# Kernel optimization log

Measured on AMD Instinct MI355X. Metric: run time of the kernel, lower is better.

Reference implementation:

```python
import jax, jax.numpy as jnp
import numpy as np

N = 8192
PERCEPTION = 0.2
SEP_DIST = 0.02
ACC_SCALE = 1.0
ACC_MAX = 1.0
EPS = 1e-08


def setup_inputs() -> dict:
    key = jax.random.key(0)
    k1, k2, k3 = jax.random.split(key, 3)
    position = jax.random.uniform(k1, (N, 2), dtype=jnp.float32)  # boids live in [0,1]^2 torus
    velocity = jax.random.normal(k2, (N, 2), dtype=jnp.float32) * 0.05
    noise = jax.random.uniform(k3, (N, 2), dtype=jnp.float32, minval=-1.0, maxval=1.0)
    return {
        "position": position,
        "velocity": velocity,
        "noise": noise,
        "separation_weight": jnp.float32(4.5),
        "alignment_weight": jnp.float32(0.65),
        "cohesion_weight": jnp.float32(0.75),
        "noise_scale": jnp.float32(0.05),
    }


def _normalize(v):
    # per-row normalize, matching module's _normalize
    norm = jnp.maximum(jnp.linalg.norm(v, axis=-1, keepdims=True), EPS)
    return v / norm


def reference(position, velocity, noise, separation_weight, alignment_weight, cohesion_weight, noise_scale):
    # Toroidal vector from boid i to boid j: diff[i, j, :]  (shape [N, N, 2])
    diff = position[None, :, :] - position[:, None, :]
    diff = jnp.where(diff > 0.5, diff - 1.0, diff)
    diff = jnp.where(diff < -0.5, diff + 1.0, diff)
    dist2 = jnp.sum(diff * diff, axis=-1)  # [N, N]

    not_self = ~jnp.eye(N, dtype=bool)

    # Separation: sum of -toroidal_vector over too-close neighbors, normalized
    sep_mask = not_self & (dist2 <= SEP_DIST ** 2)
    steer_sep = -jnp.sum(jnp.where(sep_mask[..., None], diff, 0.0), axis=1)
    steer_sep = _normalize(steer_sep)

    # Perception mask shared by alignment and cohesion
    perc_mask = not_self & (dist2 <= PERCEPTION ** 2)
    cnt = jnp.sum(perc_mask, axis=1, dtype=position.dtype)[:, None]  # [N, 1]

    # Alignment: mean neighbor velocity minus own velocity, normalized
    vel_avg = jnp.einsum("ij,jd->id", perc_mask.astype(position.dtype), velocity) / cnt
    steer_align = _normalize(vel_avg - velocity)

    # Cohesion: mean toroidal vector to neighbors, normalized
    pos_avg = jnp.sum(jnp.where(perc_mask[..., None], diff, 0.0), axis=1) / cnt
    steer_coh = _normalize(pos_avg)

    acc = (separation_weight * steer_sep
           + alignment_weight * steer_align
           + cohesion_weight * steer_coh)
    acc = acc * ACC_SCALE
    acc = acc + noise_scale * noise

    # clip by norm per boid
    norm = jnp.linalg.norm(acc, axis=-1, keepdims=True)
    acc = jnp.where(norm > ACC_MAX, acc * ACC_MAX / jnp.maximum(norm, EPS), acc)
    return acc
```

## Files before the change

### kernel.cpp

```cpp
#include <hip/hip_runtime.h>
#include <math.h>

#define N_BOIDS 8192
typedef float f32x2 __attribute__((ext_vector_type(2)));
typedef float f32x4 __attribute__((ext_vector_type(4)));

constexpr int   NC     = 16;
constexpr int   NCELL  = NC * NC;
constexpr float MARG   = 0.2002f;
constexpr int   CHUNK  = 256;
constexpr int   NBLK   = N_BOIDS / CHUNK;
constexpr size_t HIST_OFF = 0;
constexpr size_t CS_OFF   = 32768;
constexpr size_t SORT_OFF = 36864;
constexpr size_t SIDX_OFF = 167936;
constexpr size_t WS_NEED  = 200704;

constexpr float SEP_R2  = 4.0000000000000008e-04f;
constexpr float PERC_R2 = 4.0000000000000001e-02f;
constexpr float EPSF    = 1e-08f;

__device__ __forceinline__ int cell_of(float px, float py) {
    int cx = (int)(px * 16.0f); cx = cx > 15 ? 15 : (cx < 0 ? 0 : cx);
    int cy = (int)(py * 16.0f); cy = cy > 15 ? 15 : (cy < 0 ? 0 : cy);
    return cy * NC + cx;
}

__global__ __launch_bounds__(CHUNK) void cell_hist(
    const float* __restrict__ pos, int* __restrict__ hist)
{
    __shared__ int h[NCELL];
    const int tid = threadIdx.x;
    h[tid] = 0;
    __syncthreads();
    const int i = blockIdx.x * CHUNK + tid;
    atomicAdd(&h[cell_of(pos[2 * i], pos[2 * i + 1])], 1);
    __syncthreads();
    hist[blockIdx.x * NCELL + tid] = h[tid];
}

__global__ __launch_bounds__(CHUNK) void cell_scan_scatter(
    const float* __restrict__ pos, const float* __restrict__ vel,
    const int* __restrict__ hist, int* __restrict__ cs,
    float4* __restrict__ sorted4, int* __restrict__ sidx)
{
    __shared__ int tot[NCELL];
    __shared__ int lbase[NCELL];
    __shared__ int cid[CHUNK];
    const int c = threadIdx.x;
    const int b = blockIdx.x;

    int t = 0, part = 0;
#pragma unroll
    for (int bb = 0; bb < NBLK; ++bb) {
        const int hv = hist[bb * NCELL + c];
        t += hv;
        if (bb < b) part += hv;
    }
    const int mytot = t;
    tot[c] = t;
    __syncthreads();
#pragma unroll
    for (int off = 1; off < NCELL; off <<= 1) {
        int v = 0;
        if (c >= off) v = tot[c - off];
        __syncthreads();
        tot[c] += v;
        __syncthreads();
    }
    const int excl = tot[c] - mytot;
    lbase[c] = excl + part;
    cs[c] = excl;
    if (c == NCELL - 1) cs[NCELL] = tot[NCELL - 1];

    const int i = b * CHUNK + c;
    const float px = pos[2 * i], py = pos[2 * i + 1];
    const int myc = cell_of(px, py);
    cid[c] = myc;
    __syncthreads();
    int rank = 0;
    for (int t2 = 0; t2 < c; ++t2) rank += (cid[t2] == myc) ? 1 : 0;
    const int slot = lbase[myc] + rank;
    float4 o; o.x = px; o.y = py; o.z = vel[2 * i]; o.w = vel[2 * i + 1];
    sorted4[slot] = o;
    sidx[slot]    = i;
}

__device__ __forceinline__ void finalize_core(
    float vix, float viy, const f32x2 nz,
    float ws, float wa, float wc, float wn,
    float sx, float sy, float vx, float vy, float cx, float cy, float cntall,
    float* __restrict__ out, int orig)
{
    const float cnt = cntall - 1.0f;
    float ns  = fmaxf(sqrtf(sx * sx + sy * sy), EPSF);
    float ssx = sx / ns, ssy = sy / ns;
    float vax = (vx - vix) / cnt - vix;
    float vay = (vy - viy) / cnt - viy;
    float na  = fmaxf(sqrtf(vax * vax + vay * vay), EPSF);
    float sax = vax / na, say = vay / na;
    float pax = cx / cnt, pay = cy / cnt;
    float nc  = fmaxf(sqrtf(pax * pax + pay * pay), EPSF);
    float scx = pax / nc, scy = pay / nc;
    float ax = ws * ssx + wa * sax + wc * scx;
    float ay = ws * ssy + wa * say + wc * scy;
    ax += wn * nz.x;
    ay += wn * nz.y;
    const float nn = sqrtf(ax * ax + ay * ay);
    if (nn > 1.0f) {
        const float s = 1.0f / fmaxf(nn, EPSF);
        ax *= s;
        ay *= s;
    }
    out[2 * orig]     = ax;
    out[2 * orig + 1] = ay;
}

__global__ __launch_bounds__(256, 8) void boids_main(
    const float4* __restrict__ sorted4,
    const int* __restrict__ sidx,
    const int* __restrict__ cs,
    const f32x2* __restrict__ noise,
    const float* __restrict__ w_sep,
    const float* __restrict__ w_ali,
    const float* __restrict__ w_coh,
    const float* __restrict__ w_noise,
    float* __restrict__ out)
{
    __shared__ int cs_l[NCELL + 1];
    const int tid = threadIdx.x;
    cs_l[tid] = cs[tid];
    if (tid == 0) cs_l[NCELL] = cs[NCELL];
    __syncthreads();

    const int lane = tid & 63;
    const int wid  = tid >> 6;
    const int si   = blockIdx.x * 4 + wid;

    const float4 I0 = sorted4[si];
    const float vperc = PERC_R2;
    const float vsep  = SEP_R2;

    const int cx0 = (int)floorf((I0.x - MARG) * 16.0f);
    const int cx1 = (int)floorf((I0.x + MARG) * 16.0f);
    const int cy0 = (int)floorf((I0.y - MARG) * 16.0f);
    const int cy1 = (int)floorf((I0.y + MARG) * 16.0f);
    int nx = cx1 - cx0 + 1; if (nx > NC) nx = NC;
    int ny = cy1 - cy0 + 1; if (ny > NC) ny = NC;
    const int a0 = cx0 & (NC - 1);
    const int lenA = (nx < NC - a0) ? nx : (NC - a0);
    const int lenB = nx - lenA;

    float n0 = 0.f, s0x = 0.f, s0y = 0.f, v0x = 0.f, v0y = 0.f, c0x = 0.f, c0y = 0.f;

    for (int r = 0; r < ny; ++r) {
        const int ry      = (cy0 + r) & (NC - 1);
        const int rowbase = ry * NC;
        const int sA = cs_l[rowbase + a0];
        const int eA = cs_l[rowbase + a0 + lenA];
        const int sB = cs_l[rowbase];
        const int eB = cs_l[rowbase + lenB];
        for (int seg = 0; seg < 2; ++seg) {
            const int js = seg ? sB : sA;
            const int je = seg ? eB : eA;
            for (int j0 = js; j0 < je; j0 += 64) {
                const int   rem = je - j0;
                const int   jj  = (lane < rem) ? (j0 + lane) : j0;
                const float inv = (lane < rem) ? 0.0f : 1e9f;
                const float4 q  = sorted4[jj];
                float dx, dy, ta, tb, m;
                asm(
                    "v_sub_f32   %[dx], %[qx], %[px]\n\t"
                    "v_sub_f32   %[dy], %[qy], %[py]\n\t"
                    "v_rndne_f32 %[ta], %[dx]\n\t"
                    "v_rndne_f32 %[tb], %[dy]\n\t"
                    "v_sub_f32   %[dx], %[dx], %[ta]\n\t"
                    "v_sub_f32   %[dy], %[dy], %[tb]\n\t"
                    "v_mul_f32   %[ta], %[dx], %[dx]\n\t"
                    "v_mul_f32   %[tb], %[dy], %[dy]\n\t"
                    "v_add_f32   %[ta], %[ta], %[tb]\n\t"
                    "v_max_f32   %[ta], %[ta], %[inv]\n\t"
                    "v_cmp_ge_f32 vcc, %[vperc], %[ta]\n\t"
                    "v_cndmask_b32 %[m], 0, 1.0, vcc\n\t"
                    "v_add_f32   %[n0], %[n0], %[m]\n\t"
                    "v_fmac_f32  %[v0x], %[m], %[qz]\n\t"
                    "v_fmac_f32  %[v0y], %[m], %[qw]\n\t"
                    "v_fmac_f32  %[c0x], %[m], %[dx]\n\t"
                    "v_fmac_f32  %[c0y], %[m], %[dy]\n\t"
                    "v_cmp_ge_f32 vcc, %[vsep], %[ta]\n\t"
                    "v_cndmask_b32 %[m], 0, 1.0, vcc\n\t"
                    "v_fma_f32   %[s0x], -%[m], %[dx], %[s0x]\n\t"
                    "v_fma_f32   %[s0y], -%[m], %[dy], %[s0y]\n\t"
                    : [dx] "=&v"(dx), [dy] "=&v"(dy), [ta] "=&v"(ta),
                      [tb] "=&v"(tb), [m] "=&v"(m),
                      [n0] "+v"(n0), [s0x] "+v"(s0x), [s0y] "+v"(s0y),
                      [v0x] "+v"(v0x), [v0y] "+v"(v0y),
                      [c0x] "+v"(c0x), [c0y] "+v"(c0y)
                    : [qx] "v"(q.x), [qy] "v"(q.y), [qz] "v"(q.z), [qw] "v"(q.w),
                      [px] "v"(I0.x), [py] "v"(I0.y),
                      [vperc] "v"(vperc), [vsep] "v"(vsep), [inv] "v"(inv)
                    : "vcc");
            }
        }
    }

#pragma unroll
    for (int mlev = 1; mlev < 64; mlev <<= 1) {
        n0  += __shfl_xor(n0,  mlev);
        s0x += __shfl_xor(s0x, mlev);  s0y += __shfl_xor(s0y, mlev);
        v0x += __shfl_xor(v0x, mlev);  v0y += __shfl_xor(v0y, mlev);
        c0x += __shfl_xor(c0x, mlev);  c0y += __shfl_xor(c0y, mlev);
    }

    if (lane == 0) {
        const int orig = sidx[si];
        finalize_core(I0.z, I0.w, noise[orig],
                      w_sep[0], w_ali[0], w_coh[0], w_noise[0],
                      s0x, s0y, v0x, v0y, c0x, c0y, n0, out, orig);
    }
}

constexpr int FB_BLOCK = 256;
constexpr int FB_TILE  = 2048;

__global__ __launch_bounds__(FB_BLOCK, 4) void boids_allpairs(
    const f32x2* __restrict__ pos, const f32x2* __restrict__ vel,
    const f32x2* __restrict__ noise,
    const float* __restrict__ w_sep, const float* __restrict__ w_ali,
    const float* __restrict__ w_coh, const float* __restrict__ w_noise,
    float* __restrict__ out)
{
    __shared__ f32x4 tile[FB_TILE];
    const int tid  = threadIdx.x;
    const int lane = tid & 63;
    const int wid  = tid >> 6;
    const int i0   = (blockIdx.x * 4 + wid) * 2;
    const f32x2 P0 = pos[i0];
    const f32x2 P1 = pos[i0 + 1];
    const float vperc = PERC_R2, vsep = SEP_R2;
    float n0 = 0.f, s0x = 0.f, s0y = 0.f, v0x = 0.f, v0y = 0.f, c0x = 0.f, c0y = 0.f;
    float n1 = 0.f, s1x = 0.f, s1y = 0.f, v1x = 0.f, v1y = 0.f, c1x = 0.f, c1y = 0.f;
    for (int t = 0; t < N_BOIDS / FB_TILE; ++t) {
        const f32x4* gp = reinterpret_cast<const f32x4*>(pos) + t * (FB_TILE / 2);
        const f32x4* gv = reinterpret_cast<const f32x4*>(vel) + t * (FB_TILE / 2);
#pragma unroll
        for (int c = 0; c < FB_TILE / 2 / FB_BLOCK; ++c) {
            const int idx  = tid + c * FB_BLOCK;
            const f32x4 pp = gp[idx];
            const f32x4 vv = gv[idx];
            f32x4 t0; t0.x = pp.x; t0.y = pp.y; t0.z = vv.x; t0.w = vv.y;
            f32x4 t1; t1.x = pp.z; t1.y = pp.w; t1.z = vv.z; t1.w = vv.w;
            tile[2 * idx] = t0; tile[2 * idx + 1] = t1;
        }
        __syncthreads();
#pragma unroll 8
        for (int k = 0; k < FB_TILE / 64; ++k) {
            const f32x4 q = tile[lane + k * 64];
            float dx, dy, ta, tb, m;
            asm("v_sub_f32 %[dx], %[qx], %[p0x]\n\t"
                "v_sub_f32 %[dy], %[qy], %[p0y]\n\t"
                "v_rndne_f32 %[ta], %[dx]\n\t"
                "v_rndne_f32 %[tb], %[dy]\n\t"
                "v_sub_f32 %[dx], %[dx], %[ta]\n\t"
                "v_sub_f32 %[dy], %[dy], %[tb]\n\t"
                "v_mul_f32 %[ta], %[dx], %[dx]\n\t"
                "v_mul_f32 %[tb], %[dy], %[dy]\n\t"
                "v_add_f32 %[ta], %[ta], %[tb]\n\t"
                "v_cmp_ge_f32 vcc, %[vperc], %[ta]\n\t"
                "v_cndmask_b32 %[m], 0, 1.0, vcc\n\t"
                "v_add_f32 %[n0], %[n0], %[m]\n\t"
                "v_fmac_f32 %[v0x], %[m], %[qz]\n\t"
                "v_fmac_f32 %[v0y], %[m], %[qw]\n\t"
                "v_fmac_f32 %[c0x], %[m], %[dx]\n\t"
                "v_fmac_f32 %[c0y], %[m], %[dy]\n\t"
                "v_cmp_ge_f32 vcc, %[vsep], %[ta]\n\t"
                "v_cndmask_b32 %[m], 0, 1.0, vcc\n\t"
                "v_fma_f32 %[s0x], -%[m], %[dx], %[s0x]\n\t"
                "v_fma_f32 %[s0y], -%[m], %[dy], %[s0y]\n\t"
                "v_sub_f32 %[dx], %[qx], %[p1x]\n\t"
                "v_sub_f32 %[dy], %[qy], %[p1y]\n\t"
                "v_rndne_f32 %[ta], %[dx]\n\t"
                "v_rndne_f32 %[tb], %[dy]\n\t"
                "v_sub_f32 %[dx], %[dx], %[ta]\n\t"
                "v_sub_f32 %[dy], %[dy], %[tb]\n\t"
                "v_mul_f32 %[ta], %[dx], %[dx]\n\t"
                "v_mul_f32 %[tb], %[dy], %[dy]\n\t"
                "v_add_f32 %[ta], %[ta], %[tb]\n\t"
                "v_cmp_ge_f32 vcc, %[vperc], %[ta]\n\t"
                "v_cndmask_b32 %[m], 0, 1.0, vcc\n\t"
                "v_add_f32 %[n1], %[n1], %[m]\n\t"
                "v_fmac_f32 %[v1x], %[m], %[qz]\n\t"
                "v_fmac_f32 %[v1y], %[m], %[qw]\n\t"
                "v_fmac_f32 %[c1x], %[m], %[dx]\n\t"
                "v_fmac_f32 %[c1y], %[m], %[dy]\n\t"
                "v_cmp_ge_f32 vcc, %[vsep], %[ta]\n\t"
                "v_cndmask_b32 %[m], 0, 1.0, vcc\n\t"
                "v_fma_f32 %[s1x], -%[m], %[dx], %[s1x]\n\t"
                "v_fma_f32 %[s1y], -%[m], %[dy], %[s1y]\n\t"
                : [dx] "=&v"(dx), [dy] "=&v"(dy), [ta] "=&v"(ta),
                  [tb] "=&v"(tb), [m] "=&v"(m),
                  [n0] "+v"(n0), [s0x] "+v"(s0x), [s0y] "+v"(s0y),
                  [v0x] "+v"(v0x), [v0y] "+v"(v0y), [c0x] "+v"(c0x), [c0y] "+v"(c0y),
                  [n1] "+v"(n1), [s1x] "+v"(s1x), [s1y] "+v"(s1y),
                  [v1x] "+v"(v1x), [v1y] "+v"(v1y), [c1x] "+v"(c1x), [c1y] "+v"(c1y)
                : [qx] "v"(q.x), [qy] "v"(q.y), [qz] "v"(q.z), [qw] "v"(q.w),
                  [p0x] "v"(P0.x), [p0y] "v"(P0.y),
                  [p1x] "v"(P1.x), [p1y] "v"(P1.y),
                  [vperc] "v"(vperc), [vsep] "v"(vsep)
                : "vcc");
        }
        __syncthreads();
    }
#pragma unroll
    for (int mlev = 1; mlev < 64; mlev <<= 1) {
        n0  += __shfl_xor(n0,  mlev);
        s0x += __shfl_xor(s0x, mlev);  s0y += __shfl_xor(s0y, mlev);
        v0x += __shfl_xor(v0x, mlev);  v0y += __shfl_xor(v0y, mlev);
        c0x += __shfl_xor(c0x, mlev);  c0y += __shfl_xor(c0y, mlev);
        n1  += __shfl_xor(n1,  mlev);
        s1x += __shfl_xor(s1x, mlev);  s1y += __shfl_xor(s1y, mlev);
        v1x += __shfl_xor(v1x, mlev);  v1y += __shfl_xor(v1y, mlev);
        c1x += __shfl_xor(c1x, mlev);  c1y += __shfl_xor(c1y, mlev);
    }
    if (lane < 2) {
        float sx = s0x, sy = s0y, vx = v0x, vy = v0y, cx = c0x, cy = c0y, cc = n0;
        int i = i0;
        if (lane == 1) {
            sx = s1x; sy = s1y; vx = v1x; vy = v1y; cx = c1x; cy = c1y; cc = n1;
            i = i0 + 1;
        }
        finalize_core(vel[i].x, vel[i].y, noise[i],
                      w_sep[0], w_ali[0], w_coh[0], w_noise[0],
                      sx, sy, vx, vy, cx, cy, cc, out, i);
    }
}

extern "C" void kernel_launch(void* const* d_in, const int* in_sizes, int n_in,
                              void* d_out, int out_size, void* d_ws, size_t ws_size,
                              hipStream_t stream) {
    const float* pos_f   = (const float*)d_in[0];
    const float* vel_f   = (const float*)d_in[1];
    const f32x2* noise   = (const f32x2*)d_in[2];
    const float* w_sep   = (const float*)d_in[3];
    const float* w_ali   = (const float*)d_in[4];
    const float* w_coh   = (const float*)d_in[5];
    const float* w_noise = (const float*)d_in[6];
    float* out = (float*)d_out;

    if (ws_size >= WS_NEED) {
        char* wsb = (char*)d_ws;
        int*    hist    = (int*)(wsb + HIST_OFF);
        int*    cs      = (int*)(wsb + CS_OFF);
        float4* sorted4 = (float4*)(wsb + SORT_OFF);
        int*    sidx    = (int*)(wsb + SIDX_OFF);
        cell_hist<<<NBLK, CHUNK, 0, stream>>>(pos_f, hist);
        cell_scan_scatter<<<NBLK, CHUNK, 0, stream>>>(pos_f, vel_f, hist, cs,
                                                      sorted4, sidx);
        boids_main<<<N_BOIDS / 4, 256, 0, stream>>>(
            sorted4, sidx, cs, noise, w_sep, w_ali, w_coh, w_noise, out);
    } else {
        boids_allpairs<<<N_BOIDS / 8, FB_BLOCK, 0, stream>>>(
            (const f32x2*)pos_f, (const f32x2*)vel_f, noise,
            w_sep, w_ali, w_coh, w_noise, out);
    }
}
```

Measured before the change: 35.83 us.

## Process boids per grid cell with shared neighbor list staged in LDS

Merges the histogram and scan/scatter kernels into one sort kernel that has every block recount all boids, which removes a launch. The main kernel now runs one block per grid cell: it builds a circular stencil of neighbor cell segments, stages those neighbors into LDS, and lets each wave reuse every staged neighbor across up to 8 boids held in registers. Global neighbor reads drop from once per boid to once per cell. In exchange there are only 256 blocks, register pressure is higher, work per cell is uneven, and crowded cells need a slow fallback loop.

```diff
diff --git a/kernel.cpp b/kernel.cpp
--- a/kernel.cpp
+++ b/kernel.cpp
@@ -5,16 +5,16 @@
 typedef float f32x2 __attribute__((ext_vector_type(2)));
 typedef float f32x4 __attribute__((ext_vector_type(4)));
 
-constexpr int   NC     = 16;
-constexpr int   NCELL  = NC * NC;
-constexpr float MARG   = 0.2002f;
-constexpr int   CHUNK  = 256;
-constexpr int   NBLK   = N_BOIDS / CHUNK;
-constexpr size_t HIST_OFF = 0;
-constexpr size_t CS_OFF   = 32768;
-constexpr size_t SORT_OFF = 36864;
-constexpr size_t SIDX_OFF = 167936;
-constexpr size_t WS_NEED  = 200704;
+constexpr int   NC    = 16;
+constexpr int   NCELL = NC * NC;
+constexpr int   CHUNK = 256;
+constexpr int   NBLK  = N_BOIDS / CHUNK;
+constexpr int   MAXP  = 8;
+constexpr int   WLCAP = 4096;
+constexpr size_t CS_OFF   = 0;
+constexpr size_t SORT_OFF = 4096;
+constexpr size_t SIDX_OFF = 135168;
+constexpr size_t WS_NEED  = 167936;
 
 constexpr float SEP_R2  = 4.0000000000000008e-04f;
 constexpr float PERC_R2 = 4.0000000000000001e-02f;
@@ -26,64 +26,96 @@
     return cy * NC + cx;
 }
 
-__global__ __launch_bounds__(CHUNK) void cell_hist(
-    const float* __restrict__ pos, int* __restrict__ hist)
-{
-    __shared__ int h[NCELL];
-    const int tid = threadIdx.x;
-    h[tid] = 0;
-    __syncthreads();
-    const int i = blockIdx.x * CHUNK + tid;
-    atomicAdd(&h[cell_of(pos[2 * i], pos[2 * i + 1])], 1);
-    __syncthreads();
-    hist[blockIdx.x * NCELL + tid] = h[tid];
-}
-
-__global__ __launch_bounds__(CHUNK) void cell_scan_scatter(
+__global__ __launch_bounds__(CHUNK) void sort_all(
     const float* __restrict__ pos, const float* __restrict__ vel,
-    const int* __restrict__ hist, int* __restrict__ cs,
-    float4* __restrict__ sorted4, int* __restrict__ sidx)
+    int* __restrict__ cs, float4* __restrict__ sorted4, int* __restrict__ sidx)
 {
     __shared__ int tot[NCELL];
-    __shared__ int lbase[NCELL];
+    __shared__ int part[NCELL];
+    __shared__ int scan[NCELL];
     __shared__ int cid[CHUNK];
     const int c = threadIdx.x;
     const int b = blockIdx.x;
-
-    int t = 0, part = 0;
-#pragma unroll
-    for (int bb = 0; bb < NBLK; ++bb) {
-        const int hv = hist[bb * NCELL + c];
-        t += hv;
-        if (bb < b) part += hv;
-    }
-    const int mytot = t;
-    tot[c] = t;
+    tot[c] = 0; part[c] = 0;
+    __syncthreads();
+    const int lim = b * CHUNK;
+    for (int i = c; i < N_BOIDS; i += CHUNK) {
+        const int cc = cell_of(pos[2 * i], pos[2 * i + 1]);
+        atomicAdd(&tot[cc], 1);
+        if (i < lim) atomicAdd(&part[cc], 1);
+    }
+    __syncthreads();
+    scan[c] = tot[c];
     __syncthreads();
 #pragma unroll
     for (int off = 1; off < NCELL; off <<= 1) {
-        int v = 0;
-        if (c >= off) v = tot[c - off];
-        __syncthreads();
-        tot[c] += v;
-        __syncthreads();
-    }
-    const int excl = tot[c] - mytot;
-    lbase[c] = excl + part;
-    cs[c] = excl;
-    if (c == NCELL - 1) cs[NCELL] = tot[NCELL - 1];
-
-    const int i = b * CHUNK + c;
+        int v = (c >= off) ? scan[c - off] : 0;
+        __syncthreads();
+        scan[c] += v;
+        __syncthreads();
+    }
+    if (b == 0) {
+        cs[c] = scan[c] - tot[c];
+        if (c == NCELL - 1) cs[NCELL] = scan[NCELL - 1];
+    }
+    const int i = lim + c;
     const float px = pos[2 * i], py = pos[2 * i + 1];
     const int myc = cell_of(px, py);
     cid[c] = myc;
     __syncthreads();
     int rank = 0;
     for (int t2 = 0; t2 < c; ++t2) rank += (cid[t2] == myc) ? 1 : 0;
-    const int slot = lbase[myc] + rank;
+    const int slot = (scan[myc] - tot[myc]) + part[myc] + rank;
     float4 o; o.x = px; o.y = py; o.z = vel[2 * i]; o.w = vel[2 * i + 1];
     sorted4[slot] = o;
     sidx[slot]    = i;
+}
+
+__device__ __forceinline__ void pair_acc(
+    const float4& q, float px, float py, float inv,
+    float& n, float& sx, float& sy, float& vx, float& vy, float& cx, float& cy)
+{
+    float dx, dy, ta, tb, m;
+    asm("v_sub_f32   %[dx], %[qx], %[px]\n\t"
+        "v_sub_f32   %[dy], %[qy], %[py]\n\t"
+        "v_rndne_f32 %[ta], %[dx]\n\t"
+        "v_rndne_f32 %[tb], %[dy]\n\t"
+        "v_sub_f32   %[dx], %[dx], %[ta]\n\t"
+        "v_sub_f32   %[dy], %[dy], %[tb]\n\t"
+        "v_mul_f32   %[ta], %[dx], %[dx]\n\t"
+        "v_mul_f32   %[tb], %[dy], %[dy]\n\t"
+        "v_add_f32   %[ta], %[ta], %[tb]\n\t"
+        "v_max_f32   %[ta], %[ta], %[inv]\n\t"
+        "v_cmp_ge_f32 vcc, %[vperc], %[ta]\n\t"
+        "v_cndmask_b32 %[m], 0, 1.0, vcc\n\t"
+        "v_add_f32   %[n], %[n], %[m]\n\t"
+        "v_fmac_f32  %[vx], %[m], %[qz]\n\t"
+        "v_fmac_f32  %[vy], %[m], %[qw]\n\t"
+        "v_fmac_f32  %[cx], %[m], %[dx]\n\t"
+        "v_fmac_f32  %[cy], %[m], %[dy]\n\t"
+        "v_cmp_ge_f32 vcc, %[vsep], %[ta]\n\t"
+        "v_cndmask_b32 %[m], 0, 1.0, vcc\n\t"
+        "v_fma_f32   %[sx], -%[m], %[dx], %[sx]\n\t"
+        "v_fma_f32   %[sy], -%[m], %[dy], %[sy]\n\t"
+        : [dx] "=&v"(dx), [dy] "=&v"(dy), [ta] "=&v"(ta),
+          [tb] "=&v"(tb), [m] "=&v"(m),
+          [n] "+v"(n), [sx] "+v"(sx), [sy] "+v"(sy),
+          [vx] "+v"(vx), [vy] "+v"(vy), [cx] "+v"(cx), [cy] "+v"(cy)
+        : [qx] "v"(q.x), [qy] "v"(q.y), [qz] "v"(q.z), [qw] "v"(q.w),
+          [px] "v"(px), [py] "v"(py),
+          [vperc] "v"(PERC_R2), [vsep] "v"(SEP_R2), [inv] "v"(inv)
+        : "vcc");
+}
+
+__device__ __forceinline__ void bfly7(float& a, float& b, float& c, float& d,
+                                      float& e, float& f, float& g)
+{
+#pragma unroll
+    for (int m = 1; m < 64; m <<= 1) {
+        a += __shfl_xor(a, m); b += __shfl_xor(b, m); c += __shfl_xor(c, m);
+        d += __shfl_xor(d, m); e += __shfl_xor(e, m); f += __shfl_xor(f, m);
+        g += __shfl_xor(g, m);
+    }
 }
 
 __device__ __forceinline__ void finalize_core(
@@ -109,114 +141,142 @@
     const float nn = sqrtf(ax * ax + ay * ay);
     if (nn > 1.0f) {
         const float s = 1.0f / fmaxf(nn, EPSF);
-        ax *= s;
-        ay *= s;
+        ax *= s; ay *= s;
     }
     out[2 * orig]     = ax;
     out[2 * orig + 1] = ay;
 }
 
-__global__ __launch_bounds__(256, 8) void boids_main(
+__global__ __launch_bounds__(512) void boids_cell(
     const float4* __restrict__ sorted4,
     const int* __restrict__ sidx,
     const int* __restrict__ cs,
     const f32x2* __restrict__ noise,
-    const float* __restrict__ w_sep,
-    const float* __restrict__ w_ali,
-    const float* __restrict__ w_coh,
-    const float* __restrict__ w_noise,
+    const float* __restrict__ w_sep, const float* __restrict__ w_ali,
+    const float* __restrict__ w_coh, const float* __restrict__ w_noise,
     float* __restrict__ out)
 {
-    __shared__ int cs_l[NCELL + 1];
-    const int tid = threadIdx.x;
-    cs_l[tid] = cs[tid];
-    if (tid == 0) cs_l[NCELL] = cs[NCELL];
-    __syncthreads();
-
+    __shared__ int    cs_l[NCELL + 1];
+    __shared__ int    seg_src[20], seg_dst[20];
+    __shared__ int    nseg_s, total_s;
+    __shared__ float4 wl[WLCAP];
+
+    const int tid  = threadIdx.x;
     const int lane = tid & 63;
     const int wid  = tid >> 6;
-    const int si   = blockIdx.x * 4 + wid;
-
-    const float4 I0 = sorted4[si];
-    const float vperc = PERC_R2;
-    const float vsep  = SEP_R2;
-
-    const int cx0 = (int)floorf((I0.x - MARG) * 16.0f);
-    const int cx1 = (int)floorf((I0.x + MARG) * 16.0f);
-    const int cy0 = (int)floorf((I0.y - MARG) * 16.0f);
-    const int cy1 = (int)floorf((I0.y + MARG) * 16.0f);
-    int nx = cx1 - cx0 + 1; if (nx > NC) nx = NC;
-    int ny = cy1 - cy0 + 1; if (ny > NC) ny = NC;
-    const int a0 = cx0 & (NC - 1);
-    const int lenA = (nx < NC - a0) ? nx : (NC - a0);
-    const int lenB = nx - lenA;
-
-    float n0 = 0.f, s0x = 0.f, s0y = 0.f, v0x = 0.f, v0y = 0.f, c0x = 0.f, c0y = 0.f;
-
-    for (int r = 0; r < ny; ++r) {
-        const int ry      = (cy0 + r) & (NC - 1);
-        const int rowbase = ry * NC;
-        const int sA = cs_l[rowbase + a0];
-        const int eA = cs_l[rowbase + a0 + lenA];
-        const int sB = cs_l[rowbase];
-        const int eB = cs_l[rowbase + lenB];
-        for (int seg = 0; seg < 2; ++seg) {
-            const int js = seg ? sB : sA;
-            const int je = seg ? eB : eA;
+
+    for (int i = tid; i < NCELL + 1; i += 512) cs_l[i] = cs[i];
+    __syncthreads();
+
+    const int cellId = blockIdx.x;
+    const int cx = cellId & (NC - 1), cy = cellId >> 4;
+
+    if (tid == 0) {
+        const int HW[9] = {2, 3, 4, 4, 4, 4, 4, 3, 2};
+        int ns = 0, tot = 0;
+        for (int oy = -4; oy <= 4; ++oy) {
+            const int ry = (cy + oy) & (NC - 1);
+            const int rb = ry * NC;
+            const int hw = HW[oy + 4];
+            const int ncl = 2 * hw + 1;
+            const int xs = (cx - hw) & (NC - 1);
+            const int lA = (ncl < NC - xs) ? ncl : (NC - xs);
+            const int sA = cs_l[rb + xs], eA = cs_l[rb + xs + lA];
+            if (eA > sA) { seg_src[ns] = sA; seg_dst[ns] = tot; tot += eA - sA; ++ns; }
+            const int lB = ncl - lA;
+            if (lB > 0) {
+                const int sB = cs_l[rb], eB = cs_l[rb + lB];
+                if (eB > sB) { seg_src[ns] = sB; seg_dst[ns] = tot; tot += eB - sB; ++ns; }
+            }
+        }
+        nseg_s = ns; total_s = tot; seg_dst[ns] = tot;
+    }
+    __syncthreads();
+    const int nseg = nseg_s, total = total_s;
+    const int cstart = cs_l[cellId], cend = cs_l[cellId + 1];
+    const int n = cend - cstart;
+    int npass = (n - wid + 7) >> 3;
+    if (npass < 0) npass = 0;
+    if (npass > MAXP) npass = MAXP;
+
+    float Px[MAXP], Py[MAXP], Vx[MAXP], Vy[MAXP];
+    float an[MAXP], asx[MAXP], asy[MAXP], avx[MAXP], avy[MAXP], acx[MAXP], acy[MAXP];
+#pragma unroll
+    for (int p = 0; p < MAXP; ++p) {
+        Px[p] = 0.f; Py[p] = 0.f; Vx[p] = 0.f; Vy[p] = 0.f;
+        an[p] = 0.f; asx[p] = 0.f; asy[p] = 0.f;
+        avx[p] = 0.f; avy[p] = 0.f; acx[p] = 0.f; acy[p] = 0.f;
+    }
+#pragma unroll
+    for (int p = 0; p < MAXP; ++p) {
+        if (p < npass) {
+            const float4 I = sorted4[cstart + wid + p * 8];
+            Px[p] = I.x; Py[p] = I.y; Vx[p] = I.z; Vy[p] = I.w;
+        }
+    }
+
+    for (int base = 0; base < total; base += WLCAP) {
+        const int clen = (total - base < WLCAP) ? (total - base) : WLCAP;
+        for (int g = tid; g < clen; g += 512) {
+            const int gg = base + g;
+            int s = 0;
+            while (s + 1 < nseg && gg >= seg_dst[s + 1]) ++s;
+            wl[g] = sorted4[seg_src[s] + (gg - seg_dst[s])];
+        }
+        __syncthreads();
+        for (int j0 = 0; j0 < clen; j0 += 64) {
+            const int   idx = j0 + lane;
+            const float inv = (idx < clen) ? 0.0f : 1e9f;
+            const float4 q  = wl[(idx < clen) ? idx : (clen - 1)];
+#define PB(p) pair_acc(q, Px[p], Py[p], inv, an[p], asx[p], asy[p], avx[p], avy[p], acx[p], acy[p]);
+            if (npass > 0) { PB(0)
+            if (npass > 1) { PB(1)
+            if (npass > 2) { PB(2)
+            if (npass > 3) { PB(3)
+            if (npass > 4) { PB(4)
+            if (npass > 5) { PB(5)
+            if (npass > 6) { PB(6)
+            if (npass > 7) { PB(7) } } } } } } } }
+#undef PB
+        }
+        __syncthreads();
+    }
+
+    const float ws = w_sep[0], wa = w_ali[0], wc = w_coh[0], wn = w_noise[0];
+#pragma unroll
+    for (int p = 0; p < MAXP; ++p) {
+        if (p < npass) {
+            bfly7(an[p], asx[p], asy[p], avx[p], avy[p], acx[p], acy[p]);
+            if (lane == 0) {
+                const int si = cstart + wid + p * 8;
+                const int orig = sidx[si];
+                finalize_core(Vx[p], Vy[p], noise[orig], ws, wa, wc, wn,
+                              asx[p], asy[p], avx[p], avy[p], acx[p], acy[p],
+                              an[p], out, orig);
+            }
+        }
+    }
+
+    for (int p = MAXP; cstart + wid + p * 8 < cend; ++p) {
+        const int si = cstart + wid + p * 8;
+        const float4 I = sorted4[si];
+        float n2 = 0, sx = 0, sy = 0, vx = 0, vy = 0, cx2 = 0, cy2 = 0;
+        for (int s = 0; s < nseg; ++s) {
+            const int js = seg_src[s];
+            const int je = js + (seg_dst[s + 1] - seg_dst[s]);
             for (int j0 = js; j0 < je; j0 += 64) {
-                const int   rem = je - j0;
-                const int   jj  = (lane < rem) ? (j0 + lane) : j0;
-                const float inv = (lane < rem) ? 0.0f : 1e9f;
-                const float4 q  = sorted4[jj];
-                float dx, dy, ta, tb, m;
-                asm(
-                    "v_sub_f32   %[dx], %[qx], %[px]\n\t"
-                    "v_sub_f32   %[dy], %[qy], %[py]\n\t"
-                    "v_rndne_f32 %[ta], %[dx]\n\t"
-                    "v_rndne_f32 %[tb], %[dy]\n\t"
-                    "v_sub_f32   %[dx], %[dx], %[ta]\n\t"
-                    "v_sub_f32   %[dy], %[dy], %[tb]\n\t"
-                    "v_mul_f32   %[ta], %[dx], %[dx]\n\t"
-                    "v_mul_f32   %[tb], %[dy], %[dy]\n\t"
-                    "v_add_f32   %[ta], %[ta], %[tb]\n\t"
-                    "v_max_f32   %[ta], %[ta], %[inv]\n\t"
-                    "v_cmp_ge_f32 vcc, %[vperc], %[ta]\n\t"
-                    "v_cndmask_b32 %[m], 0, 1.0, vcc\n\t"
-                    "v_add_f32   %[n0], %[n0], %[m]\n\t"
-                    "v_fmac_f32  %[v0x], %[m], %[qz]\n\t"
-                    "v_fmac_f32  %[v0y], %[m], %[qw]\n\t"
-                    "v_fmac_f32  %[c0x], %[m], %[dx]\n\t"
-                    "v_fmac_f32  %[c0y], %[m], %[dy]\n\t"
-                    "v_cmp_ge_f32 vcc, %[vsep], %[ta]\n\t"
-                    "v_cndmask_b32 %[m], 0, 1.0, vcc\n\t"
-                    "v_fma_f32   %[s0x], -%[m], %[dx], %[s0x]\n\t"
-                    "v_fma_f32   %[s0y], -%[m], %[dy], %[s0y]\n\t"
-                    : [dx] "=&v"(dx), [dy] "=&v"(dy), [ta] "=&v"(ta),
-                      [tb] "=&v"(tb), [m] "=&v"(m),
-                      [n0] "+v"(n0), [s0x] "+v"(s0x), [s0y] "+v"(s0y),
-                      [v0x] "+v"(v0x), [v0y] "+v"(v0y),
-                      [c0x] "+v"(c0x), [c0y] "+v"(c0y)
-                    : [qx] "v"(q.x), [qy] "v"(q.y), [qz] "v"(q.z), [qw] "v"(q.w),
-                      [px] "v"(I0.x), [py] "v"(I0.y),
-                      [vperc] "v"(vperc), [vsep] "v"(vsep), [inv] "v"(inv)
-                    : "vcc");
+                const int   idx = j0 + lane;
+                const float inv = (idx < je) ? 0.0f : 1e9f;
+                const float4 q  = sorted4[(idx < je) ? idx : (je - 1)];
+                pair_acc(q, I.x, I.y, inv, n2, sx, sy, vx, vy, cx2, cy2);
             }
         }
-    }
-
-#pragma unroll
-    for (int mlev = 1; mlev < 64; mlev <<= 1) {
-        n0  += __shfl_xor(n0,  mlev);
-        s0x += __shfl_xor(s0x, mlev);  s0y += __shfl_xor(s0y, mlev);
-        v0x += __shfl_xor(v0x, mlev);  v0y += __shfl_xor(v0y, mlev);
-        c0x += __shfl_xor(c0x, mlev);  c0y += __shfl_xor(c0y, mlev);
-    }
-
-    if (lane == 0) {
-        const int orig = sidx[si];
-        finalize_core(I0.z, I0.w, noise[orig],
-                      w_sep[0], w_ali[0], w_coh[0], w_noise[0],
-                      s0x, s0y, v0x, v0y, c0x, c0y, n0, out, orig);
+        bfly7(n2, sx, sy, vx, vy, cx2, cy2);
+        if (lane == 0) {
+            const int orig = sidx[si];
+            finalize_core(I.z, I.w, noise[orig], ws, wa, wc, wn,
+                          sx, sy, vx, vy, cx2, cy2, n2, out, orig);
+        }
     }
 }
 
@@ -237,7 +297,6 @@
     const int i0   = (blockIdx.x * 4 + wid) * 2;
     const f32x2 P0 = pos[i0];
     const f32x2 P1 = pos[i0 + 1];
-    const float vperc = PERC_R2, vsep = SEP_R2;
     float n0 = 0.f, s0x = 0.f, s0y = 0.f, v0x = 0.f, v0y = 0.f, c0x = 0.f, c0y = 0.f;
     float n1 = 0.f, s1x = 0.f, s1y = 0.f, v1x = 0.f, v1y = 0.f, c1x = 0.f, c1y = 0.f;
     for (int t = 0; t < N_BOIDS / FB_TILE; ++t) {
@@ -255,73 +314,15 @@
         __syncthreads();
 #pragma unroll 8
         for (int k = 0; k < FB_TILE / 64; ++k) {
-            const f32x4 q = tile[lane + k * 64];
-            float dx, dy, ta, tb, m;
-            asm("v_sub_f32 %[dx], %[qx], %[p0x]\n\t"
-                "v_sub_f32 %[dy], %[qy], %[p0y]\n\t"
-                "v_rndne_f32 %[ta], %[dx]\n\t"
-                "v_rndne_f32 %[tb], %[dy]\n\t"
-                "v_sub_f32 %[dx], %[dx], %[ta]\n\t"
-                "v_sub_f32 %[dy], %[dy], %[tb]\n\t"
-                "v_mul_f32 %[ta], %[dx], %[dx]\n\t"
-                "v_mul_f32 %[tb], %[dy], %[dy]\n\t"
-                "v_add_f32 %[ta], %[ta], %[tb]\n\t"
-                "v_cmp_ge_f32 vcc, %[vperc], %[ta]\n\t"
-                "v_cndmask_b32 %[m], 0, 1.0, vcc\n\t"
-                "v_add_f32 %[n0], %[n0], %[m]\n\t"
-                "v_fmac_f32 %[v0x], %[m], %[qz]\n\t"
-                "v_fmac_f32 %[v0y], %[m], %[qw]\n\t"
-                "v_fmac_f32 %[c0x], %[m], %[dx]\n\t"
-                "v_fmac_f32 %[c0y], %[m], %[dy]\n\t"
-                "v_cmp_ge_f32 vcc, %[vsep], %[ta]\n\t"
-                "v_cndmask_b32 %[m], 0, 1.0, vcc\n\t"
-                "v_fma_f32 %[s0x], -%[m], %[dx], %[s0x]\n\t"
-                "v_fma_f32 %[s0y], -%[m], %[dy], %[s0y]\n\t"
-                "v_sub_f32 %[dx], %[qx], %[p1x]\n\t"
-                "v_sub_f32 %[dy], %[qy], %[p1y]\n\t"
-                "v_rndne_f32 %[ta], %[dx]\n\t"
-                "v_rndne_f32 %[tb], %[dy]\n\t"
-                "v_sub_f32 %[dx], %[dx], %[ta]\n\t"
-                "v_sub_f32 %[dy], %[dy], %[tb]\n\t"
-                "v_mul_f32 %[ta], %[dx], %[dx]\n\t"
-                "v_mul_f32 %[tb], %[dy], %[dy]\n\t"
-                "v_add_f32 %[ta], %[ta], %[tb]\n\t"
-                "v_cmp_ge_f32 vcc, %[vperc], %[ta]\n\t"
-                "v_cndmask_b32 %[m], 0, 1.0, vcc\n\t"
-                "v_add_f32 %[n1], %[n1], %[m]\n\t"
-                "v_fmac_f32 %[v1x], %[m], %[qz]\n\t"
-                "v_fmac_f32 %[v1y], %[m], %[qw]\n\t"
-                "v_fmac_f32 %[c1x], %[m], %[dx]\n\t"
-                "v_fmac_f32 %[c1y], %[m], %[dy]\n\t"
-                "v_cmp_ge_f32 vcc, %[vsep], %[ta]\n\t"
-                "v_cndmask_b32 %[m], 0, 1.0, vcc\n\t"
-                "v_fma_f32 %[s1x], -%[m], %[dx], %[s1x]\n\t"
-                "v_fma_f32 %[s1y], -%[m], %[dy], %[s1y]\n\t"
-                : [dx] "=&v"(dx), [dy] "=&v"(dy), [ta] "=&v"(ta),
-                  [tb] "=&v"(tb), [m] "=&v"(m),
-                  [n0] "+v"(n0), [s0x] "+v"(s0x), [s0y] "+v"(s0y),
-                  [v0x] "+v"(v0x), [v0y] "+v"(v0y), [c0x] "+v"(c0x), [c0y] "+v"(c0y),
-                  [n1] "+v"(n1), [s1x] "+v"(s1x), [s1y] "+v"(s1y),
-                  [v1x] "+v"(v1x), [v1y] "+v"(v1y), [c1x] "+v"(c1x), [c1y] "+v"(c1y)
-                : [qx] "v"(q.x), [qy] "v"(q.y), [qz] "v"(q.z), [qw] "v"(q.w),
-                  [p0x] "v"(P0.x), [p0y] "v"(P0.y),
-                  [p1x] "v"(P1.x), [p1y] "v"(P1.y),
-                  [vperc] "v"(vperc), [vsep] "v"(vsep)
-                : "vcc");
-        }
-        __syncthreads();
-    }
-#pragma unroll
-    for (int mlev = 1; mlev < 64; mlev <<= 1) {
-        n0  += __shfl_xor(n0,  mlev);
-        s0x += __shfl_xor(s0x, mlev);  s0y += __shfl_xor(s0y, mlev);
-        v0x += __shfl_xor(v0x, mlev);  v0y += __shfl_xor(v0y, mlev);
-        c0x += __shfl_xor(c0x, mlev);  c0y += __shfl_xor(c0y, mlev);
-        n1  += __shfl_xor(n1,  mlev);
-        s1x += __shfl_xor(s1x, mlev);  s1y += __shfl_xor(s1y, mlev);
-        v1x += __shfl_xor(v1x, mlev);  v1y += __shfl_xor(v1y, mlev);
-        c1x += __shfl_xor(c1x, mlev);  c1y += __shfl_xor(c1y, mlev);
-    }
+            const f32x4 qq = tile[lane + k * 64];
+            float4 q; q.x = qq.x; q.y = qq.y; q.z = qq.z; q.w = qq.w;
+            pair_acc(q, P0.x, P0.y, 0.0f, n0, s0x, s0y, v0x, v0y, c0x, c0y);
+            pair_acc(q, P1.x, P1.y, 0.0f, n1, s1x, s1y, v1x, v1y, c1x, c1y);
+        }
+        __syncthreads();
+    }
+    bfly7(n0, s0x, s0y, v0x, v0y, c0x, c0y);
+    bfly7(n1, s1x, s1y, v1x, v1y, c1x, c1y);
     if (lane < 2) {
         float sx = s0x, sy = s0y, vx = v0x, vy = v0y, cx = c0x, cy = c0y, cc = n0;
         int i = i0;
@@ -349,14 +350,11 @@
 
     if (ws_size >= WS_NEED) {
         char* wsb = (char*)d_ws;
-        int*    hist    = (int*)(wsb + HIST_OFF);
         int*    cs      = (int*)(wsb + CS_OFF);
         float4* sorted4 = (float4*)(wsb + SORT_OFF);
         int*    sidx    = (int*)(wsb + SIDX_OFF);
-        cell_hist<<<NBLK, CHUNK, 0, stream>>>(pos_f, hist);
-        cell_scan_scatter<<<NBLK, CHUNK, 0, stream>>>(pos_f, vel_f, hist, cs,
-                                                      sorted4, sidx);
-        boids_main<<<N_BOIDS / 4, 256, 0, stream>>>(
+        sort_all<<<NBLK, CHUNK, 0, stream>>>(pos_f, vel_f, cs, sorted4, sidx);
+        boids_cell<<<NCELL, 512, 0, stream>>>(
             sorted4, sidx, cs, noise, w_sep, w_ali, w_coh, w_noise, out);
     } else {
         boids_allpairs<<<N_BOIDS / 8, FB_BLOCK, 0, stream>>>(
```

Result: slower. 47.97 us (+33.9%).
